# Performance work log

Hardware: AMD Instinct MI355X
Metric: run time of the kernel (lower is better)

Reference implementation:

```python
import jax, jax.numpy as jnp
import numpy as np

BETA = 0.9       # snn.Leaky(beta=0.9)
THRESH = 1.0     # snntorch default threshold, reset_mechanism='subtract'


def setup_inputs() -> dict:
    key = jax.random.key(0)
    ks = jax.random.split(key, 7)
    B = 16384
    return {
        "x":  jax.random.normal(ks[0], (B, 1700), dtype=jnp.float32),
        "W1": jax.random.normal(ks[1], (64, 1700), dtype=jnp.float32) * 0.02,
        "b1": jax.random.normal(ks[2], (64,), dtype=jnp.float32) * 0.02,
        "W2": jax.random.normal(ks[3], (32, 64), dtype=jnp.float32) * 0.1,
        "b2": jax.random.normal(ks[4], (32,), dtype=jnp.float32) * 0.1,
        "W3": jax.random.normal(ks[5], (2, 32), dtype=jnp.float32) * 0.1,
        "b3": jax.random.normal(ks[6], (2,), dtype=jnp.float32) * 0.1,
        "num_steps": 20,
    }


def _lif_step(mem, cur):
    # snntorch Leaky: reset (subtract) based on previous mem crossing threshold,
    # then leaky integration of the new input current.
    reset = (mem > THRESH).astype(mem.dtype)
    return BETA * mem + cur - reset * THRESH


def reference(x, W1, b1, W2, b2, W3, b3, num_steps):
    B = x.shape[0]
    # Dropout is identity in eval mode; x is constant across steps, so cur1 is
    # loop-invariant and computed once (same math as the original loop).
    cur1 = x @ W1.T + b1                         # [B, 64]

    def step(carry, _):
        mem1, mem2 = carry
        mem1 = _lif_step(mem1, cur1)             # [B, 64]
        cur2 = mem1 @ W2.T + b2                  # [B, 32]
        mem2 = _lif_step(mem2, cur2)             # [B, 32]
        return (mem1, mem2), None

    init = (jnp.zeros((B, 64), x.dtype), jnp.zeros((B, 32), x.dtype))
    (mem1, mem2), _ = jax.lax.scan(step, init, None, length=num_steps)
    return mem2 @ W3.T + b3                      # [B, 2]
```

## Files before the change

### kernel.cpp

```cpp
#include <hip/hip_runtime.h>
#include <hip/hip_bf16.h>

typedef float f32x4 __attribute__((ext_vector_type(4)));
typedef short bf16x8 __attribute__((ext_vector_type(8)));
typedef _Float16 f16x8 __attribute__((ext_vector_type(8)));

#define MFMA16  __builtin_amdgcn_mfma_f32_16x16x32_bf16
#define MFMA16F __builtin_amdgcn_mfma_f32_16x16x32_f16

static constexpr int KDIM = 1700;
static constexpr int NKT2 = 56;
static constexpr float BETA = 0.9f;
static constexpr float THRESH = 1.0f;

__device__ __forceinline__ void split_bf(float f, short& hi, short& lo) {
    __hip_bfloat16 h = __float2bfloat16(f);
    float r = f - __bfloat162float(h);
    __hip_bfloat16 l = __float2bfloat16(r);
    hi = (short)__builtin_bit_cast(unsigned short, h);
    lo = (short)__builtin_bit_cast(unsigned short, l);
}

__device__ __forceinline__ void split8(f32x4 a, f32x4 b, bf16x8& hi, bf16x8& lo) {
    #pragma unroll
    for (int i = 0; i < 4; ++i) { short h, l; split_bf(a[i], h, l); hi[i] = h; lo[i] = l; }
    #pragma unroll
    for (int i = 0; i < 4; ++i) { short h, l; split_bf(b[i], h, l); hi[4 + i] = h; lo[4 + i] = l; }
}

__device__ __forceinline__ void split8h(f32x4 a, f32x4 b, f16x8& hi, f16x8& lo) {
    #pragma unroll
    for (int i = 0; i < 4; ++i) {
        _Float16 h = (_Float16)a[i];
        hi[i] = h; lo[i] = (_Float16)(a[i] - (float)h);
    }
    #pragma unroll
    for (int i = 0; i < 4; ++i) {
        _Float16 h = (_Float16)b[i];
        hi[4 + i] = h; lo[4 + i] = (_Float16)(b[i] - (float)h);
    }
}

__global__ void w1_relayout(const float* __restrict__ W1, _Float16* __restrict__ WT) {
    const int g    = blockIdx.x * 256 + threadIdx.x;
    const int kt   = g >> 8;
    const int nt   = (g >> 6) & 3;
    const int lane = g & 63;
    const int n    = nt * 16 + (lane & 15);
    const int kb   = kt * 32 + (lane >> 4) * 8;
    f16x8 v;
    #pragma unroll
    for (int i = 0; i < 8; ++i) {
        const int k = kb + i;
        v[i] = (k < KDIM) ? (_Float16)W1[n * KDIM + k] : (_Float16)0.f;
    }
    *(f16x8*)(WT + (size_t)g * 8) = v;
}

__device__ __forceinline__ void gll16(const void* src, const void* lds_dst) {
    __builtin_amdgcn_global_load_lds(
        (const __attribute__((address_space(1))) unsigned int*)src,
        (__attribute__((address_space(3))) unsigned int*)lds_dst, 16, 0, 0);
}

__global__ __launch_bounds__(256, 2) void snn_fused(
    const float* __restrict__ x, const _Float16* __restrict__ WT,
    const float* __restrict__ b1, const float* __restrict__ W2,
    const float* __restrict__ b2, const float* __restrict__ W3,
    const float* __restrict__ b3, const int* __restrict__ nsp,
    float* __restrict__ out)
{
    __shared__ __align__(16) char smemraw[34816];
    _Float16* ldsW = (_Float16*)smemraw;
    float (*red)[32][68] = (float (*)[32][68])smemraw;

    const int tid = threadIdx.x;
    const int wid = tid >> 6;
    const int lane = tid & 63;
    const int l15 = lane & 15;
    const int g4  = lane >> 4;
    const int kg  = g4 * 8;
    const int rowBase = blockIdx.x * 32;
    const int t0  = wid * 14;

    const float* xr0 = x + (size_t)(rowBase + l15) * KDIM;
    const float* xr1 = xr0 + (size_t)16 * KDIM;
    const _Float16* pW = WT + (size_t)t0 * 2048 + lane * 8;
    _Float16* myLds = ldsW + wid * 4096;

    struct XB { f32x4 a0, a1, b0, b1; };
    auto xload = [&](int t, XB& xb) {
        const int k1 = t * 32 + kg;
        const int kc1 = (k1 <= 1696) ? k1 : 1664;
        const int kc2 = (k1 + 4 <= 1696) ? k1 + 4 : 1664;
        const float* p0 = xr0 + kc1;
        const float* p1 = xr0 + kc2;
        const float* p2 = xr1 + kc1;
        const float* p3 = xr1 + kc2;
        asm volatile("global_load_dwordx4 %0, %1, off" : "=v"(xb.a0) : "v"(p0));
        asm volatile("global_load_dwordx4 %0, %1, off" : "=v"(xb.a1) : "v"(p1));
        asm volatile("global_load_dwordx4 %0, %1, off" : "=v"(xb.b0) : "v"(p2));
        asm volatile("global_load_dwordx4 %0, %1, off" : "=v"(xb.b1) : "v"(p3));
    };
    auto stageW = [&](int i, int buf) {
        _Float16* dstb = myLds + buf * 2048;
        #pragma unroll
        for (int q = 0; q < 4; ++q)
            gll16(pW + (size_t)i * 2048 + q * 512, dstb + q * 512);
    };

    f32x4 acc[2][4] = {};
    XB x0, x1, x2;

    stageW(0, 0);
    xload(t0 + 0, x0);
    xload(t0 + 1, x1);
    stageW(1, 1);
    xload(t0 + 2, x2);

#define GSTEP(I, XC, WAITN)                                                    \
    {                                                                          \
        asm volatile("s_waitcnt vmcnt(" #WAITN ")" ::: "memory");              \
        __builtin_amdgcn_sched_barrier(0);                                     \
        const _Float16* rb = myLds + ((I) & 1) * 2048;                         \
        f16x8 WC[4];                                                           \
        _Pragma("unroll")                                                      \
        for (int q = 0; q < 4; ++q)                                            \
            WC[q] = *(const f16x8*)(rb + q * 512 + lane * 8);                  \
        f16x8 ah0, al0, ah1, al1;                                              \
        split8h(XC.a0, XC.a1, ah0, al0);                                       \
        split8h(XC.b0, XC.b1, ah1, al1);                                       \
        asm volatile("s_waitcnt lgkmcnt(0)" ::: "memory");                     \
        __builtin_amdgcn_sched_barrier(0);                                     \
        if constexpr ((I) + 2 < 14) stageW((I) + 2, (I) & 1);                  \
        if constexpr ((I) + 3 < 14) xload(t0 + (I) + 3, XC);                   \
        __builtin_amdgcn_sched_barrier(0);                                     \
        _Pragma("unroll")                                                      \
        for (int nt = 0; nt < 4; ++nt) {                                       \
            acc[0][nt] = MFMA16F(ah0, WC[nt], acc[0][nt], 0, 0, 0);            \
            acc[0][nt] = MFMA16F(al0, WC[nt], acc[0][nt], 0, 0, 0);            \
            acc[1][nt] = MFMA16F(ah1, WC[nt], acc[1][nt], 0, 0, 0);            \
            acc[1][nt] = MFMA16F(al1, WC[nt], acc[1][nt], 0, 0, 0);            \
        }                                                                      \
    }

    GSTEP(0,  x0, 12)
    GSTEP(1,  x1, 12)
    GSTEP(2,  x2, 12)
    GSTEP(3,  x0, 12)
    GSTEP(4,  x1, 12)
    GSTEP(5,  x2, 12)
    GSTEP(6,  x0, 12)
    GSTEP(7,  x1, 12)
    GSTEP(8,  x2, 12)
    GSTEP(9,  x0, 12)
    GSTEP(10, x1, 12)
    GSTEP(11, x2, 12)
    GSTEP(12, x0, 8)
    GSTEP(13, x1, 0)
#undef GSTEP

    __syncthreads();

    #pragma unroll
    for (int mt = 0; mt < 2; ++mt)
        #pragma unroll
        for (int nt = 0; nt < 4; ++nt)
            #pragma unroll
            for (int j = 0; j < 4; ++j)
                red[wid][mt * 16 + g4 * 4 + j][nt * 16 + l15] = acc[mt][nt][j];
    __syncthreads();

    {
        const int rr  = tid >> 3;
        const int seg = tid & 7;
        f32x4 s0 = *(const f32x4*)(b1 + seg * 8);
        f32x4 s1 = *(const f32x4*)(b1 + seg * 8 + 4);
        #pragma unroll
        for (int p = 0; p < 4; ++p) {
            s0 += *(const f32x4*)&red[p][rr][seg * 8];
            s1 += *(const f32x4*)&red[p][rr][seg * 8 + 4];
        }
        *(f32x4*)&red[0][rr][seg * 8]     = s0;
        *(f32x4*)&red[0][rr][seg * 8 + 4] = s1;
    }
    __syncthreads();
    if (wid >= 2) return;

    const int lrow = wid * 16 + l15;

    float c1[2][8], c1m1[2][8];
    #pragma unroll
    for (int kt = 0; kt < 2; ++kt) {
        f32x4 u0 = *(const f32x4*)&red[0][lrow][kt * 32 + kg];
        f32x4 u1 = *(const f32x4*)&red[0][lrow][kt * 32 + kg + 4];
        #pragma unroll
        for (int i = 0; i < 4; ++i) {
            c1[kt][i] = u0[i];     c1[kt][4 + i] = u1[i];
            c1m1[kt][i] = u0[i] - THRESH; c1m1[kt][4 + i] = u1[i] - THRESH;
        }
    }

    bf16x8 W2hf[2][2], W2lf[2][2];
    #pragma unroll
    for (int rt = 0; rt < 2; ++rt)
        #pragma unroll
        for (int kt = 0; kt < 2; ++kt) {
            const float* wp = W2 + (rt * 16 + l15) * 64 + kt * 32 + kg;
            split8(*(const f32x4*)wp, *(const f32x4*)(wp + 4), W2hf[rt][kt], W2lf[rt][kt]);
        }

    float b2v[2][4], b2m1[2][4], w3a[2][4], w3b[2][4];
    #pragma unroll
    for (int nt = 0; nt < 2; ++nt)
        #pragma unroll
        for (int j = 0; j < 4; ++j) {
            const int o = nt * 16 + g4 * 4 + j;
            b2v[nt][j]  = b2[o];
            b2m1[nt][j] = b2[o] - THRESH;
            w3a[nt][j] = W3[o];
            w3b[nt][j] = W3[32 + o];
        }

    float m1[2][8] = {};
    float m2[2][4] = {};
    const int ns = nsp[0];
    for (int s = 0; s < ns; ++s) {
        bf16x8 mh[2], ml[2];
        #pragma unroll
        for (int kt = 0; kt < 2; ++kt)
            #pragma unroll
            for (int i = 0; i < 8; ++i) {
                float m = m1[kt][i];
                m = __builtin_fmaf(BETA, m, (m > THRESH) ? c1m1[kt][i] : c1[kt][i]);
                m1[kt][i] = m;
                short h, l; split_bf(m, h, l);
                mh[kt][i] = h; ml[kt][i] = l;
            }
        f32x4 a2[2][2] = {};
        #pragma unroll
        for (int rt = 0; rt < 2; ++rt)
            #pragma unroll
            for (int kt = 0; kt < 2; ++kt) {
                a2[rt][kt] = MFMA16(W2hf[rt][kt], mh[kt], a2[rt][kt], 0, 0, 0);
                a2[rt][kt] = MFMA16(W2lf[rt][kt], mh[kt], a2[rt][kt], 0, 0, 0);
                a2[rt][kt] = MFMA16(W2hf[rt][kt], ml[kt], a2[rt][kt], 0, 0, 0);
            }
        #pragma unroll
        for (int nt = 0; nt < 2; ++nt) {
            f32x4 c2 = a2[nt][0] + a2[nt][1];
            #pragma unroll
            for (int j = 0; j < 4; ++j) {
                float m = m2[nt][j];
                m2[nt][j] = __builtin_fmaf(
                    BETA, m, c2[j] + ((m > THRESH) ? b2m1[nt][j] : b2v[nt][j]));
            }
        }
    }

    float p0 = 0.f, p1 = 0.f;
    #pragma unroll
    for (int nt = 0; nt < 2; ++nt)
        #pragma unroll
        for (int j = 0; j < 4; ++j) {
            p0 = __builtin_fmaf(m2[nt][j], w3a[nt][j], p0);
            p1 = __builtin_fmaf(m2[nt][j], w3b[nt][j], p1);
        }
    p0 += __shfl_xor(p0, 16); p0 += __shfl_xor(p0, 32);
    p1 += __shfl_xor(p1, 16); p1 += __shfl_xor(p1, 32);
    if (lane < 16) {
        const size_t row = rowBase + lrow;
        out[row * 2 + 0] = p0 + b3[0];
        out[row * 2 + 1] = p1 + b3[1];
    }
}

extern "C" void kernel_launch(void* const* d_in, const int* in_sizes, int n_in,
                              void* d_out, int out_size, void* d_ws, size_t ws_size,
                              hipStream_t stream) {
    const float* x  = (const float*)d_in[0];
    const float* W1 = (const float*)d_in[1];
    const float* b1 = (const float*)d_in[2];
    const float* W2 = (const float*)d_in[3];
    const float* b2 = (const float*)d_in[4];
    const float* W3 = (const float*)d_in[5];
    const float* b3 = (const float*)d_in[6];
    const int*   ns = (const int*)d_in[7];
    float* o = (float*)d_out;

    const int B = in_sizes[0] / KDIM;
    _Float16* WT = (_Float16*)d_ws;

    w1_relayout<<<NKT2, 256, 0, stream>>>(W1, WT);
    snn_fused<<<B / 32, 256, 0, stream>>>(x, WT, b1, W2, b2, W3, b3, ns, o);
}
```

Baseline: 40.61 us.

## Enlarge row tile to 64 with 512-thread blocks and 8-way K split

Each block now handles 64 rows with 8 waves, and each wave covers 7 K-tiles instead of 14, with 4 row groups per wave. Every staged W1 tile is reused across twice as many rows, which cuts LDS weight traffic per row, and the grid halves. The cost is more accumulator and x-buffer registers per wave, double LDS per block, a shallower x prefetch (2 buffers instead of 3) and a two-phase cross-wave reduction. With a single block per CU at occupancy 1, latency hiding may suffer.

```diff
diff --git a/kernel.cpp b/kernel.cpp
--- a/kernel.cpp
+++ b/kernel.cpp
@@ -63,16 +63,16 @@
         (__attribute__((address_space(3))) unsigned int*)lds_dst, 16, 0, 0);
 }
 
-__global__ __launch_bounds__(256, 2) void snn_fused(
+__global__ __launch_bounds__(512, 1) void snn_fused(
     const float* __restrict__ x, const _Float16* __restrict__ WT,
     const float* __restrict__ b1, const float* __restrict__ W2,
     const float* __restrict__ b2, const float* __restrict__ W3,
     const float* __restrict__ b3, const int* __restrict__ nsp,
     float* __restrict__ out)
 {
-    __shared__ __align__(16) char smemraw[34816];
+    __shared__ __align__(16) char smemraw[69632];
     _Float16* ldsW = (_Float16*)smemraw;
-    float (*red)[32][68] = (float (*)[32][68])smemraw;
+    float (*red)[64][68] = (float (*)[64][68])smemraw;
 
     const int tid = threadIdx.x;
     const int wid = tid >> 6;
@@ -80,27 +80,25 @@
     const int l15 = lane & 15;
     const int g4  = lane >> 4;
     const int kg  = g4 * 8;
-    const int rowBase = blockIdx.x * 32;
-    const int t0  = wid * 14;
-
-    const float* xr0 = x + (size_t)(rowBase + l15) * KDIM;
-    const float* xr1 = xr0 + (size_t)16 * KDIM;
-    const _Float16* pW = WT + (size_t)t0 * 2048 + lane * 8;
+    const int rowBase = blockIdx.x * 64;
+    const int tb  = wid * 7;
+
+    const _Float16* pW = WT + (size_t)tb * 2048 + lane * 8;
     _Float16* myLds = ldsW + wid * 4096;
 
-    struct XB { f32x4 a0, a1, b0, b1; };
+    struct XB { f32x4 v[8]; };
     auto xload = [&](int t, XB& xb) {
         const int k1 = t * 32 + kg;
         const int kc1 = (k1 <= 1696) ? k1 : 1664;
         const int kc2 = (k1 + 4 <= 1696) ? k1 + 4 : 1664;
-        const float* p0 = xr0 + kc1;
-        const float* p1 = xr0 + kc2;
-        const float* p2 = xr1 + kc1;
-        const float* p3 = xr1 + kc2;
-        asm volatile("global_load_dwordx4 %0, %1, off" : "=v"(xb.a0) : "v"(p0));
-        asm volatile("global_load_dwordx4 %0, %1, off" : "=v"(xb.a1) : "v"(p1));
-        asm volatile("global_load_dwordx4 %0, %1, off" : "=v"(xb.b0) : "v"(p2));
-        asm volatile("global_load_dwordx4 %0, %1, off" : "=v"(xb.b1) : "v"(p3));
+        #pragma unroll
+        for (int rg = 0; rg < 4; ++rg) {
+            const float* xr = x + (size_t)(rowBase + rg * 16 + l15) * KDIM;
+            const float* p0 = xr + kc1;
+            const float* p1 = xr + kc2;
+            asm volatile("global_load_dwordx4 %0, %1, off" : "=v"(xb.v[2*rg])   : "v"(p0));
+            asm volatile("global_load_dwordx4 %0, %1, off" : "=v"(xb.v[2*rg+1]) : "v"(p1));
+        }
     };
     auto stageW = [&](int i, int buf) {
         _Float16* dstb = myLds + buf * 2048;
@@ -109,14 +107,11 @@
             gll16(pW + (size_t)i * 2048 + q * 512, dstb + q * 512);
     };
 
-    f32x4 acc[2][4] = {};
-    XB x0, x1, x2;
-
-    stageW(0, 0);
-    xload(t0 + 0, x0);
-    xload(t0 + 1, x1);
-    stageW(1, 1);
-    xload(t0 + 2, x2);
+    f32x4 acc[4][4] = {};
+    XB x0, x1;
+
+    stageW(0, 0); xload(tb + 0, x0);
+    stageW(1, 1); xload(tb + 1, x1);
 
 #define GSTEP(I, XC, WAITN)                                                    \
     {                                                                          \
@@ -127,50 +122,57 @@
         _Pragma("unroll")                                                      \
         for (int q = 0; q < 4; ++q)                                            \
             WC[q] = *(const f16x8*)(rb + q * 512 + lane * 8);                  \
-        f16x8 ah0, al0, ah1, al1;                                              \
-        split8h(XC.a0, XC.a1, ah0, al0);                                       \
-        split8h(XC.b0, XC.b1, ah1, al1);                                       \
+        f16x8 ah[4], al[4];                                                    \
+        _Pragma("unroll")                                                      \
+        for (int rg = 0; rg < 4; ++rg)                                         \
+            split8h(XC.v[2*rg], XC.v[2*rg+1], ah[rg], al[rg]);                 \
         asm volatile("s_waitcnt lgkmcnt(0)" ::: "memory");                     \
         __builtin_amdgcn_sched_barrier(0);                                     \
-        if constexpr ((I) + 2 < 14) stageW((I) + 2, (I) & 1);                  \
-        if constexpr ((I) + 3 < 14) xload(t0 + (I) + 3, XC);                   \
+        if constexpr ((I) + 2 < 7) { stageW((I) + 2, (I) & 1);                 \
+                                     xload(tb + (I) + 2, XC); }                \
         __builtin_amdgcn_sched_barrier(0);                                     \
         _Pragma("unroll")                                                      \
-        for (int nt = 0; nt < 4; ++nt) {                                       \
-            acc[0][nt] = MFMA16F(ah0, WC[nt], acc[0][nt], 0, 0, 0);            \
-            acc[0][nt] = MFMA16F(al0, WC[nt], acc[0][nt], 0, 0, 0);            \
-            acc[1][nt] = MFMA16F(ah1, WC[nt], acc[1][nt], 0, 0, 0);            \
-            acc[1][nt] = MFMA16F(al1, WC[nt], acc[1][nt], 0, 0, 0);            \
-        }                                                                      \
-    }
-
-    GSTEP(0,  x0, 12)
-    GSTEP(1,  x1, 12)
-    GSTEP(2,  x2, 12)
-    GSTEP(3,  x0, 12)
-    GSTEP(4,  x1, 12)
-    GSTEP(5,  x2, 12)
-    GSTEP(6,  x0, 12)
-    GSTEP(7,  x1, 12)
-    GSTEP(8,  x2, 12)
-    GSTEP(9,  x0, 12)
-    GSTEP(10, x1, 12)
-    GSTEP(11, x2, 12)
-    GSTEP(12, x0, 8)
-    GSTEP(13, x1, 0)
+        for (int mt = 0; mt < 4; ++mt)                                         \
+            _Pragma("unroll")                                                  \
+            for (int nt = 0; nt < 4; ++nt) {                                   \
+                acc[mt][nt] = MFMA16F(ah[mt], WC[nt], acc[mt][nt], 0, 0, 0);   \
+                acc[mt][nt] = MFMA16F(al[mt], WC[nt], acc[mt][nt], 0, 0, 0);   \
+            }                                                                  \
+    }
+
+    GSTEP(0, x0, 12)
+    GSTEP(1, x1, 12)
+    GSTEP(2, x0, 12)
+    GSTEP(3, x1, 12)
+    GSTEP(4, x0, 12)
+    GSTEP(5, x1, 12)
+    GSTEP(6, x0, 0)
 #undef GSTEP
 
     __syncthreads();
-
-    #pragma unroll
-    for (int mt = 0; mt < 2; ++mt)
-        #pragma unroll
-        for (int nt = 0; nt < 4; ++nt)
-            #pragma unroll
-            for (int j = 0; j < 4; ++j)
-                red[wid][mt * 16 + g4 * 4 + j][nt * 16 + l15] = acc[mt][nt][j];
-    __syncthreads();
-
+    if (wid >= 4) {
+        #pragma unroll
+        for (int mt = 0; mt < 4; ++mt)
+            #pragma unroll
+            for (int nt = 0; nt < 4; ++nt)
+                #pragma unroll
+                for (int j = 0; j < 4; ++j)
+                    red[wid - 4][mt * 16 + g4 * 4 + j][nt * 16 + l15] = acc[mt][nt][j];
+    }
+    __syncthreads();
+    if (wid < 4) {
+        #pragma unroll
+        for (int mt = 0; mt < 4; ++mt)
+            #pragma unroll
+            for (int nt = 0; nt < 4; ++nt)
+                #pragma unroll
+                for (int j = 0; j < 4; ++j) {
+                    float v = acc[mt][nt][j]
+                            + red[wid][mt * 16 + g4 * 4 + j][nt * 16 + l15];
+                    red[wid][mt * 16 + g4 * 4 + j][nt * 16 + l15] = v;
+                }
+    }
+    __syncthreads();
     {
         const int rr  = tid >> 3;
         const int seg = tid & 7;
@@ -185,7 +187,7 @@
         *(f32x4*)&red[0][rr][seg * 8 + 4] = s1;
     }
     __syncthreads();
-    if (wid >= 2) return;
+    if (wid >= 4) return;
 
     const int lrow = wid * 16 + l15;
 
@@ -292,5 +294,5 @@
     _Float16* WT = (_Float16*)d_ws;
 
     w1_relayout<<<NKT2, 256, 0, stream>>>(W1, WT);
-    snn_fused<<<B / 32, 256, 0, stream>>>(x, WT, b1, W2, b2, W3, b3, ns, o);
-}
+    snn_fused<<<B / 64, 512, 0, stream>>>(x, WT, b1, W2, b2, W3, b3, ns, o);
+}
```

Result: no change. 40.58 us (-0.1%).
